# Performance work log

Measured on AMD Instinct MI355X. Metric: run time of the kernel, lower is better.

Reference implementation:

```python
import jax, jax.numpy as jnp
import numpy as np

NEG_RATIO = 5          # neg_sample_ratio, also k (num_nodes-1 >> ratio)
THRESH = 0.7           # hard_neg_threshold
SMOOTH = 0.1           # label_smoothing
NUM_NODES = 200_000
DIM = 128
B = 1024               # batch size, all labels == 1 (all positives)
FILL_VAL = -1.0e9


def _l2_normalize(x, eps=1e-12):
    # F.normalize(p=2, dim=-1): divide by clamped L2 norm
    n = jnp.sqrt(jnp.sum(x * x, axis=-1, keepdims=True))
    return x / jnp.maximum(n, eps)


def setup_inputs() -> dict:
    key = jax.random.key(0)
    k1, k2, k3, k4 = jax.random.split(key, 4)
    src_nodes = jax.random.randint(k1, (B,), 0, NUM_NODES)
    dst_nodes = jax.random.randint(k2, (B,), 0, NUM_NODES)
    labels = jnp.ones((B,), dtype=jnp.float32)  # all positives -> pos_mask all True
    timestamps = jax.random.uniform(k3, (B,), dtype=jnp.float32)
    memory = jax.random.normal(k4, (NUM_NODES, DIM), dtype=jnp.float32)
    return {
        "src_nodes": src_nodes,
        "dst_nodes": dst_nodes,
        "labels": labels,
        "timestamps": timestamps,
        "memory": memory,
    }


def reference(src_nodes, dst_nodes, labels, timestamps, memory):
    # --- embedding gather + L2 normalize ---
    src_emb = memory[src_nodes]                      # [B, D]
    s = _l2_normalize(src_emb).astype(jnp.float16)   # use_half_precision=True
    c = _l2_normalize(memory).astype(jnp.float16)    # [N, D]

    # --- similarity [B, N], back to fp32 ---
    sim = jnp.matmul(s, c.T).astype(jnp.float32)

    # --- mask out ground-truth dst and below-threshold sims ---
    cols = jnp.arange(NUM_NODES)
    allowed = cols[None, :] != dst_nodes[:, None]    # exclude GT positives
    valid = allowed & (sim > THRESH)
    score = jnp.where(valid, sim, FILL_VAL)

    # --- top-k hard negatives per positive ---
    k = NEG_RATIO  # min(neg_sample_ratio, num_nodes-1)
    topk_vals, topk_idx = jax.lax.top_k(score, k)    # [B, k]
    is_real = (topk_vals > FILL_VAL + 1.0).reshape(-1)  # [B*k]

    # --- fallback random negatives (fixed-shape equivalent of the torch
    #     pack-real-then-pad-random assembly; total count == B*k either way) ---
    rkey = jax.random.key(42)
    rand_dst = jax.random.randint(rkey, (B * k,), 0, NUM_NODES)
    src_rep = jnp.repeat(src_nodes, k)               # [B*k]
    rand_dst = jnp.where(rand_dst == src_rep, (rand_dst + 1) % NUM_NODES, rand_dst)

    final_src = src_rep
    final_dst = jnp.where(is_real, topk_idx.reshape(-1), rand_dst)
    neg_ts = jnp.repeat(timestamps, k)

    # --- assemble augmented batch ---
    new_src = jnp.concatenate([src_nodes, final_src])
    new_dst = jnp.concatenate([dst_nodes, final_dst])
    new_labels = jnp.concatenate([labels, jnp.zeros((B * k,), labels.dtype)])
    new_ts = jnp.concatenate([timestamps, neg_ts])

    # --- label smoothing ---
    new_labels = new_labels * (1.0 - SMOOTH) + (1.0 - new_labels) * SMOOTH

    return new_src, new_dst, new_labels, new_ts, topk_vals
```

## Files before the change

kernel.cpp:

```cpp
#include <hip/hip_runtime.h>

#define NUM_NODES 200000
#define DIM 128
#define BATCH 1024
#define K_NEG 5
#define CAP 16
#define JW 64
#define BN (4 * JW)
#define JBLOCKS 782
#define THRESH 0.7f
#define FILL (-1.0e9f)

typedef __attribute__((ext_vector_type(16))) float f32x16;

__device__ __forceinline__ unsigned char f2fp8(float x) {
  unsigned u = __builtin_bit_cast(unsigned, x);
  unsigned char s = (unsigned char)((u >> 24) & 0x80u);
  float ax = fabsf(x);
  unsigned char enc;
  if (ax < 0.015625f) {
    enc = (unsigned char)(int)rintf(ax * 512.0f);
  } else {
    int ee; float fr = frexpf(ax, &ee);
    int E = ee + 6;
    int mant = (int)rintf((fr * 2.0f - 1.0f) * 8.0f);
    enc = (unsigned char)((E << 3) + mant);
  }
  return (unsigned char)(enc | s);
}

__device__ __forceinline__ void tf2x32(unsigned k0, unsigned k1,
                                       unsigned x0, unsigned x1,
                                       unsigned* o0, unsigned* o1) {
  unsigned ks2 = k0 ^ k1 ^ 0x1BD11BDAu;
  unsigned v0 = x0 + k0, v1 = x1 + k1;
#define TFR(r) { v0 += v1; v1 = (v1 << r) | (v1 >> (32 - r)); v1 ^= v0; }
  TFR(13) TFR(15) TFR(26) TFR(6)   v0 += k1;  v1 += ks2 + 1u;
  TFR(17) TFR(29) TFR(16) TFR(24)  v0 += ks2; v1 += k0 + 2u;
  TFR(13) TFR(15) TFR(26) TFR(6)   v0 += k0;  v1 += k1 + 3u;
  TFR(17) TFR(29) TFR(16) TFR(24)  v0 += k1;  v1 += ks2 + 4u;
  TFR(13) TFR(15) TFR(26) TFR(6)   v0 += ks2; v1 += k0 + 5u;
#undef TFR
  *o0 = v0; *o1 = v1;
}

__device__ __forceinline__ unsigned rbits32(unsigned ka, unsigned kb, unsigned m) {
  unsigned o0, o1;
  tf2x32(ka, kb, 0u, m, &o0, &o1);
  return o0 ^ o1;
}


__global__ void prep_a_kernel(const float* __restrict__ memory,
                              const int* __restrict__ src_nodes,
                              unsigned char* __restrict__ afragA,
                              int* __restrict__ cand_cnt) {
  int tid = threadIdx.x;
  int gid = blockIdx.x * 256 + tid;
  if (gid < BATCH) cand_cnt[gid] = 0;
  int row = blockIdx.x * 4 + (tid >> 6);
  int L = tid & 63;
  int s = src_nodes[row];
  float2 v = ((const float2*)(memory + (size_t)s * DIM))[L];
  float ss = v.x * v.x + v.y * v.y;
#pragma unroll
  for (int off = 32; off > 0; off >>= 1) ss += __shfl_xor(ss, off);
  float inv = 1.0f / fmaxf(sqrtf(ss), 1e-12f);
  unsigned char b0 = f2fp8(v.x * inv), b1 = f2fp8(v.y * inv);
  int ms = row >> 5, l32 = row & 31;
  int c = 2 * L;
  int kp = c >> 5, half = (c >> 3) & 1, tp = ((c >> 4) & 1) * 8 + (c & 7);
  size_t chunk = ((size_t)(ms * 4 + kp)) * 64 + half * 32 + l32;
  *(unsigned short*)(afragA + chunk * 16 + tp) =
      (unsigned short)((unsigned)b0 | ((unsigned)b1 << 8));
}

__global__ void prep_c_kernel(const float* __restrict__ memory,
                              unsigned long long* __restrict__ cfrag) {
  int tid = threadIdx.x;
  int wid = tid >> 6;
  int lane = tid & 63;
  int half = lane >> 5;
  int l32 = lane & 31;
  int rowbase = blockIdx.x * BN + wid * 64;
#pragma unroll
  for (int js = 0; js < 2; ++js) {
    int j = rowbase + js * 32 + l32;
    bool jv = (j < NUM_NODES);
    const float4* rp4 = (const float4*)(memory + (size_t)j * DIM);
    float4 q[16];
#pragma unroll
    for (int ks = 0; ks < 8; ++ks) {
      q[ks * 2]     = jv ? rp4[ks * 4 + half * 2]     : make_float4(0.f, 0.f, 0.f, 0.f);
      q[ks * 2 + 1] = jv ? rp4[ks * 4 + half * 2 + 1] : make_float4(0.f, 0.f, 0.f, 0.f);
    }
    float ss = 0.0f;
#pragma unroll
    for (int i = 0; i < 16; ++i)
      ss += q[i].x * q[i].x + q[i].y * q[i].y + q[i].z * q[i].z + q[i].w * q[i].w;
    ss += __shfl_xor(ss, 32);
    float inv = 1.0f / fmaxf(sqrtf(ss), 1e-12f);
#pragma unroll
    for (int ks = 0; ks < 8; ++ks) {
      float4 a = q[ks * 2], b = q[ks * 2 + 1];
      unsigned long long w =
          (unsigned long long)f2fp8(a.x * inv)
        | ((unsigned long long)f2fp8(a.y * inv) << 8)
        | ((unsigned long long)f2fp8(a.z * inv) << 16)
        | ((unsigned long long)f2fp8(a.w * inv) << 24)
        | ((unsigned long long)f2fp8(b.x * inv) << 32)
        | ((unsigned long long)f2fp8(b.y * inv) << 40)
        | ((unsigned long long)f2fp8(b.z * inv) << 48)
        | ((unsigned long long)f2fp8(b.w * inv) << 56);
      cfrag[((size_t)(j >> 5) * 8 + ks) * 64 + half * 32 + l32] = w;
    }
  }
}

__global__ __launch_bounds__(256, 4) void sim_scan_kernel(
    const ulong2* __restrict__ afragG,
    const unsigned long long* __restrict__ cfrag,
    const int* __restrict__ dst_nodes,
    int* __restrict__ cand_cnt,
    float* __restrict__ cand_val,
    int* __restrict__ cand_idx) {
  __shared__ ulong2 aT[2048];
  int tid = threadIdx.x;
  int wid = tid >> 6;
  int lane = tid & 63;
  int half = lane >> 5;
  int l32 = lane & 31;
  int jb = blockIdx.x * BN + wid * JW;

  long bf[2][8];
#pragma unroll
  for (int js = 0; js < 2; ++js)
#pragma unroll
    for (int ks = 0; ks < 8; ++ks)
      bf[js][ks] = (long)cfrag[((size_t)((jb >> 5) + js) * 8 + ks) * 64 + lane];

  for (int p = 0; p < 4; ++p) {
    __syncthreads();
    const ulong2* g = afragG + p * 2048;
#pragma unroll
    for (int c = 0; c < 8; ++c) {
      int idx = c * 256 + tid;
      aT[idx] = g[idx];
    }
    __syncthreads();

#pragma unroll
    for (int ml = 0; ml < 8; ++ml) {
      int ms = p * 8 + ml;
      ulong2 av[4];
#pragma unroll
      for (int kp = 0; kp < 4; ++kp) av[kp] = aT[(ml * 4 + kp) * 64 + lane];
      f32x16 acc0, acc1;
#pragma unroll
      for (int i = 0; i < 16; ++i) { acc0[i] = 0.0f; acc1[i] = 0.0f; }
#pragma unroll
      for (int kp = 0; kp < 4; ++kp) {
        long alo = (long)av[kp].x;
        long ahi = (long)av[kp].y;
        acc0 = __builtin_amdgcn_mfma_f32_32x32x16_fp8_fp8(alo, bf[0][2 * kp], acc0, 0, 0, 0);
        acc1 = __builtin_amdgcn_mfma_f32_32x32x16_fp8_fp8(alo, bf[1][2 * kp], acc1, 0, 0, 0);
        acc0 = __builtin_amdgcn_mfma_f32_32x32x16_fp8_fp8(ahi, bf[0][2 * kp + 1], acc0, 0, 0, 0);
        acc1 = __builtin_amdgcn_mfma_f32_32x32x16_fp8_fp8(ahi, bf[1][2 * kp + 1], acc1, 0, 0, 0);
      }
      float m[16];
#pragma unroll
      for (int i = 0; i < 16; ++i) m[i] = fmaxf(acc0[i], acc1[i]);
#pragma unroll
      for (int i = 0; i < 8; ++i) m[i] = fmaxf(m[i], m[i + 8]);
#pragma unroll
      for (int i = 0; i < 4; ++i) m[i] = fmaxf(m[i], m[i + 4]);
      float vm = fmaxf(fmaxf(m[0], m[1]), fmaxf(m[2], m[3]));
      if (vm > THRESH) {
#pragma unroll
        for (int js = 0; js < 2; ++js) {
          int gj = jb + js * 32 + l32;
#pragma unroll
          for (int r = 0; r < 16; ++r) {
            float v = (js == 0) ? acc0[r] : acc1[r];
            if (v > THRESH) {
              int gi = ms * 32 + (r & 3) + 8 * (r >> 2) + 4 * half;
              if (gj < NUM_NODES && gj != dst_nodes[gi]) {
                int pp = atomicAdd(&cand_cnt[gi], 1);
                if (pp < CAP) {
                  cand_val[gi * CAP + pp] = v;
                  cand_idx[gi * CAP + pp] = gj;
                }
              }
            }
          }
        }
      }
    }
  }
}

__global__ void finalize_kernel(const int* __restrict__ src_nodes,
                                const int* __restrict__ dst_nodes,
                                const float* __restrict__ labels,
                                const float* __restrict__ ts,
                                const int* __restrict__ cand_cnt,
                                const float* __restrict__ cand_val,
                                const int* __restrict__ cand_idx,
                                float* __restrict__ out) {
  int r = blockIdx.x * 256 + threadIdx.x;
  if (r >= BATCH) return;
  const int TOT = BATCH + BATCH * K_NEG;
  int srcv = src_nodes[r];
  float tsv = ts[r];
  out[r] = (float)srcv;
  out[TOT + r] = (float)dst_nodes[r];
  float l = labels[r];
  out[2 * TOT + r] = l * 0.9f + (1.0f - l) * 0.1f;
  out[3 * TOT + r] = tsv;

  int cnt = cand_cnt[r];
  cnt = cnt < CAP ? cnt : CAP;
  float cv[CAP]; int ci[CAP];
  for (int i = 0; i < cnt; ++i) { cv[i] = cand_val[r * CAP + i]; ci[i] = cand_idx[r * CAP + i]; }

  unsigned k1a, k1b, k2a, k2b;
  tf2x32(0u, 42u, 0u, 0u, &k1a, &k1b);
  tf2x32(0u, 42u, 0u, 1u, &k2a, &k2b);

  const unsigned span = 200000u;
  const unsigned mult = 167296u;

  for (int s = 0; s < K_NEG; ++s) {
    int sel = -1;
    for (int i = 0; i < cnt; ++i)
      if (sel < 0 || cv[i] > cv[sel] || (cv[i] == cv[sel] && ci[i] < ci[sel])) sel = i;
    float v = FILL; int idx = 0;
    if (sel >= 0) { v = cv[sel]; idx = ci[sel]; cv[sel] = FILL; ci[sel] = 0x7fffffff; }
    bool is_real = v > (FILL + 1.0f);

    unsigned m = (unsigned)(r * K_NEG + s);
    unsigned hi = rbits32(k1a, k1b, m);
    unsigned lo = rbits32(k2a, k2b, m);
    unsigned off = ((hi % span) * mult + (lo % span)) % span;
    int rd = (int)off;
    if (rd == srcv) rd = (rd + 1) % NUM_NODES;
    int fd = is_real ? idx : rd;

    int mi = (int)m;
    out[BATCH + mi] = (float)srcv;
    out[TOT + BATCH + mi] = (float)fd;
    out[2 * TOT + BATCH + mi] = 0.1f;
    out[3 * TOT + BATCH + mi] = tsv;
    out[4 * TOT + mi] = v;
  }
}

extern "C" void kernel_launch(void* const* d_in, const int* in_sizes, int n_in,
                              void* d_out, int out_size, void* d_ws, size_t ws_size,
                              hipStream_t stream) {
  const int* src = (const int*)d_in[0];
  const int* dst = (const int*)d_in[1];
  const float* labels = (const float*)d_in[2];
  const float* ts = (const float*)d_in[3];
  const float* memory = (const float*)d_in[4];
  float* out = (float*)d_out;

  char* ws = (char*)d_ws;
  unsigned long long* cfrag = (unsigned long long*)ws;
  size_t off = (size_t)JBLOCKS * 256 * 128;
  unsigned char* afragA = (unsigned char*)(ws + off);
  int* cand_cnt = (int*)(ws + off + 131072);
  float* cand_val = (float*)(ws + off + 135168);
  int* cand_idx = (int*)(ws + off + 200704);

  prep_a_kernel<<<256, 256, 0, stream>>>(memory, src, afragA, cand_cnt);
  prep_c_kernel<<<JBLOCKS, 256, 0, stream>>>(memory, cfrag);
  sim_scan_kernel<<<JBLOCKS, 256, 0, stream>>>((const ulong2*)afragA, cfrag, dst,
                                               cand_cnt, cand_val, cand_idx);
  finalize_kernel<<<(BATCH + 255) / 256, 256, 0, stream>>>(src, dst, labels, ts,
                                                           cand_cnt, cand_val, cand_idx, out);
}
```

Measured before the change: 227.0 us.

## Fuse candidate normalization and FP8 packing into the similarity scan kernel

Result: slower. 276.5 us (+21.8%).

```diff
diff --git a/kernel.cpp b/kernel.cpp
--- a/kernel.cpp
+++ b/kernel.cpp
@@ -75,51 +75,9 @@
       (unsigned short)((unsigned)b0 | ((unsigned)b1 << 8));
 }
 
-__global__ void prep_c_kernel(const float* __restrict__ memory,
-                              unsigned long long* __restrict__ cfrag) {
-  int tid = threadIdx.x;
-  int wid = tid >> 6;
-  int lane = tid & 63;
-  int half = lane >> 5;
-  int l32 = lane & 31;
-  int rowbase = blockIdx.x * BN + wid * 64;
-#pragma unroll
-  for (int js = 0; js < 2; ++js) {
-    int j = rowbase + js * 32 + l32;
-    bool jv = (j < NUM_NODES);
-    const float4* rp4 = (const float4*)(memory + (size_t)j * DIM);
-    float4 q[16];
-#pragma unroll
-    for (int ks = 0; ks < 8; ++ks) {
-      q[ks * 2]     = jv ? rp4[ks * 4 + half * 2]     : make_float4(0.f, 0.f, 0.f, 0.f);
-      q[ks * 2 + 1] = jv ? rp4[ks * 4 + half * 2 + 1] : make_float4(0.f, 0.f, 0.f, 0.f);
-    }
-    float ss = 0.0f;
-#pragma unroll
-    for (int i = 0; i < 16; ++i)
-      ss += q[i].x * q[i].x + q[i].y * q[i].y + q[i].z * q[i].z + q[i].w * q[i].w;
-    ss += __shfl_xor(ss, 32);
-    float inv = 1.0f / fmaxf(sqrtf(ss), 1e-12f);
-#pragma unroll
-    for (int ks = 0; ks < 8; ++ks) {
-      float4 a = q[ks * 2], b = q[ks * 2 + 1];
-      unsigned long long w =
-          (unsigned long long)f2fp8(a.x * inv)
-        | ((unsigned long long)f2fp8(a.y * inv) << 8)
-        | ((unsigned long long)f2fp8(a.z * inv) << 16)
-        | ((unsigned long long)f2fp8(a.w * inv) << 24)
-        | ((unsigned long long)f2fp8(b.x * inv) << 32)
-        | ((unsigned long long)f2fp8(b.y * inv) << 40)
-        | ((unsigned long long)f2fp8(b.z * inv) << 48)
-        | ((unsigned long long)f2fp8(b.w * inv) << 56);
-      cfrag[((size_t)(j >> 5) * 8 + ks) * 64 + half * 32 + l32] = w;
-    }
-  }
-}
-
 __global__ __launch_bounds__(256, 4) void sim_scan_kernel(
+    const float* __restrict__ memory,
     const ulong2* __restrict__ afragG,
-    const unsigned long long* __restrict__ cfrag,
     const int* __restrict__ dst_nodes,
     int* __restrict__ cand_cnt,
     float* __restrict__ cand_val,
@@ -134,10 +92,36 @@
 
   long bf[2][8];
 #pragma unroll
-  for (int js = 0; js < 2; ++js)
-#pragma unroll
-    for (int ks = 0; ks < 8; ++ks)
-      bf[js][ks] = (long)cfrag[((size_t)((jb >> 5) + js) * 8 + ks) * 64 + lane];
+  for (int js = 0; js < 2; ++js) {
+    int j = jb + js * 32 + l32;
+    bool jv = (j < NUM_NODES);
+    const float4* rp4 = (const float4*)(memory + (size_t)j * DIM);
+    float4 q[16];
+#pragma unroll
+    for (int ks = 0; ks < 8; ++ks) {
+      q[ks * 2]     = jv ? rp4[ks * 4 + half * 2]     : make_float4(0.f, 0.f, 0.f, 0.f);
+      q[ks * 2 + 1] = jv ? rp4[ks * 4 + half * 2 + 1] : make_float4(0.f, 0.f, 0.f, 0.f);
+    }
+    float ss = 0.0f;
+#pragma unroll
+    for (int i = 0; i < 16; ++i)
+      ss += q[i].x * q[i].x + q[i].y * q[i].y + q[i].z * q[i].z + q[i].w * q[i].w;
+    ss += __shfl_xor(ss, 32);
+    float inv = 1.0f / fmaxf(sqrtf(ss), 1e-12f);
+#pragma unroll
+    for (int ks = 0; ks < 8; ++ks) {
+      float4 a = q[ks * 2], b = q[ks * 2 + 1];
+      unsigned lo = (unsigned)f2fp8(a.x * inv)
+                  | ((unsigned)f2fp8(a.y * inv) << 8)
+                  | ((unsigned)f2fp8(a.z * inv) << 16)
+                  | ((unsigned)f2fp8(a.w * inv) << 24);
+      unsigned hi = (unsigned)f2fp8(b.x * inv)
+                  | ((unsigned)f2fp8(b.y * inv) << 8)
+                  | ((unsigned)f2fp8(b.z * inv) << 16)
+                  | ((unsigned)f2fp8(b.w * inv) << 24);
+      bf[js][ks] = (long)(((unsigned long long)hi << 32) | lo);
+    }
+  }
 
   for (int p = 0; p < 4; ++p) {
     __syncthreads();
@@ -266,16 +250,13 @@
   float* out = (float*)d_out;
 
   char* ws = (char*)d_ws;
-  unsigned long long* cfrag = (unsigned long long*)ws;
-  size_t off = (size_t)JBLOCKS * 256 * 128;
-  unsigned char* afragA = (unsigned char*)(ws + off);
-  int* cand_cnt = (int*)(ws + off + 131072);
-  float* cand_val = (float*)(ws + off + 135168);
-  int* cand_idx = (int*)(ws + off + 200704);
+  unsigned char* afragA = (unsigned char*)ws;
+  int* cand_cnt = (int*)(ws + 131072);
+  float* cand_val = (float*)(ws + 135168);
+  int* cand_idx = (int*)(ws + 200704);
 
   prep_a_kernel<<<256, 256, 0, stream>>>(memory, src, afragA, cand_cnt);
-  prep_c_kernel<<<JBLOCKS, 256, 0, stream>>>(memory, cfrag);
-  sim_scan_kernel<<<JBLOCKS, 256, 0, stream>>>((const ulong2*)afragA, cfrag, dst,
+  sim_scan_kernel<<<JBLOCKS, 256, 0, stream>>>(memory, (const ulong2*)afragA, dst,
                                                cand_cnt, cand_val, cand_idx);
   finalize_kernel<<<(BATCH + 255) / 256, 256, 0, stream>>>(src, dst, labels, ts,
                                                            cand_cnt, cand_val, cand_idx, out);
```
